# Kernel optimization log

Hardware: AMD Instinct MI355X
Metric: run time of the kernel (lower is better)

## Reference

```python
import jax, jax.numpy as jnp
import numpy as np

N, M = 8192, 4096
SCALE = 1e-4  # keeps tss ~ O(1) so the gaussian score doesn't underflow


def setup_inputs() -> dict:
    key = jax.random.key(0)
    x = jax.random.normal(key, (N, M), dtype=jnp.float32) * SCALE
    variance = jnp.asarray(0.9, dtype=jnp.float32)
    return {"x": x, "variance": variance}


def reference(x, variance):
    # _lpd vectorized over all columns at once.
    # series_a/series_b are first differences with a leading zero row; the
    # leading zeros contribute 0 to the sum (0*0>=0 -> 0-0), so we can work
    # directly on the diffs.
    d = jnp.diff(x, axis=0)                 # [N-1, M]
    da = d[:, :1]                           # reference column diffs [N-1, 1]
    db = d[:, 1:]                           # other column diffs    [N-1, M-1]
    diff = da - db
    hpdd = jnp.where(da * db >= 0, diff, jnp.abs(diff))
    tss = jnp.sum(hpdd, axis=0)             # [M-1]
    # torch.tensor(self.tss) detaches tss from x's autograd graph
    tss = jax.lax.stop_gradient(tss)

    # gaussian score with mean 0, sigma = variance
    sqrt_2pi = jnp.sqrt(jnp.asarray(2.0 * np.pi, dtype=x.dtype))
    coef = 1.0 / (sqrt_2pi * variance)
    score = coef * jnp.exp(-(tss ** 2) / (2.0 * variance ** 2))  # [M-1]

    # tan-softmax weighting
    t = jnp.tan(score)
    w = t / jnp.sum(t)                      # [M-1]

    y = jnp.reshape(jnp.sum(w * x[:, 1:]), (-1,))  # [1]
    return y
```

## Files before the change

kernel.cpp:

```cpp
#include <hip/hip_runtime.h>
#include <math.h>

#define NROWS 8192
#define NCOLS 4096
#define RPC 64
#define NCHUNK (NROWS / RPC)
#define TPB 256
#define CPT 4
#define CTILE (TPB * CPT)
#define NTILE (NCOLS / CTILE)
#define F2BLK 64
#define CPB2 (NCOLS / F2BLK)

typedef float f32x4 __attribute__((ext_vector_type(4)));

__global__ __launch_bounds__(TPB) void tss_partial_kernel(
    const float* __restrict__ x,
    float* __restrict__ ptss,
    float* __restrict__ pcs)
{
    const int tid   = threadIdx.x;
    const int tile  = blockIdx.x;
    const int chunk = blockIdx.y;
    const int col   = tile * CTILE + tid * CPT;
    const int r0    = chunk * RPC;

    __shared__ float x0[RPC + 1];
    __shared__ float da_sh[RPC];

    if (tid <= RPC) {
        int r = min(r0 + tid, NROWS - 1);
        x0[tid] = x[(size_t)r * NCOLS];
    }
    __syncthreads();
    if (tid < RPC) {
        da_sh[tid] = (r0 + tid + 1 < NROWS) ? (x0[tid + 1] - x0[tid]) : 0.0f;
    }
    __syncthreads();

    const f32x4* row = (const f32x4*)(x + (size_t)r0 * NCOLS + col);
    const int rs = NCOLS / 4;
    const int maxoff = NROWS - 1 - r0;

    float tss0 = 0.f, tss1 = 0.f, tss2 = 0.f, tss3 = 0.f;
    float cs0 = 0.f, cs1 = 0.f, cs2 = 0.f, cs3 = 0.f;

    f32x4 cur = row[0];
    f32x4 nxt = row[rs];

    #pragma unroll 8
    for (int i = 0; i < RPC; ++i) {
        const int offc = (i + 2 <= RPC) ? (i + 2) : RPC;
        const int off  = min(offc, maxoff);
        f32x4 pf = row[off * rs];

        cs0 += cur.x; cs1 += cur.y; cs2 += cur.z; cs3 += cur.w;

        const float da = da_sh[i];
        float db, df;
        db = nxt.x - cur.x; df = da - db;
        tss0 += (da * db >= 0.f) ? df : fabsf(df);
        db = nxt.y - cur.y; df = da - db;
        tss1 += (da * db >= 0.f) ? df : fabsf(df);
        db = nxt.z - cur.z; df = da - db;
        tss2 += (da * db >= 0.f) ? df : fabsf(df);
        db = nxt.w - cur.w; df = da - db;
        tss3 += (da * db >= 0.f) ? df : fabsf(df);

        cur = nxt;
        nxt = pf;
    }

    float* pt = ptss + (size_t)chunk * NCOLS + col;
    float* pc = pcs  + (size_t)chunk * NCOLS + col;
    pt[0] = tss0; pt[1] = tss1; pt[2] = tss2; pt[3] = tss3;
    pc[0] = cs0;  pc[1] = cs1;  pc[2] = cs2;  pc[3] = cs3;
}

__global__ __launch_bounds__(256) void tss_finalize_kernel(
    const float* __restrict__ ptss,
    const float* __restrict__ pcs,
    const float* __restrict__ variance,
    double* __restrict__ blk)
{
    const int tid  = threadIdx.x;
    const int part = tid >> 6;
    const int cpos = tid & 63;
    const int j    = blockIdx.x * CPB2 + cpos;

    double tss = 0.0, cs = 0.0;
    #pragma unroll 8
    for (int c = part * (NCHUNK / 4); c < (part + 1) * (NCHUNK / 4); ++c) {
        tss += (double)ptss[(size_t)c * NCOLS + j];
        cs  += (double)pcs[(size_t)c * NCOLS + j];
    }

    __shared__ double stss[4][CPB2];
    __shared__ double scs[4][CPB2];
    stss[part][cpos] = tss;
    scs[part][cpos]  = cs;
    __syncthreads();

    if (tid < 64) {
        tss = stss[0][cpos] + stss[1][cpos] + stss[2][cpos] + stss[3][cpos];
        cs  = scs[0][cpos] + scs[1][cpos] + scs[2][cpos] + scs[3][cpos];

        double t = 0.0, tc = 0.0;
        if (j >= 1) {
            const double var = (double)variance[0];
            const double SQRT_2PI = 2.5066282746310005024;
            const double coef = 1.0 / (SQRT_2PI * var);
            const double score = coef * exp(-(tss * tss) / (2.0 * var * var));
            t  = tan(score);
            tc = t * cs;
        }
        for (int o = 32; o > 0; o >>= 1) {
            t  += __shfl_down(t, o);
            tc += __shfl_down(tc, o);
        }
        if (cpos == 0) {
            blk[2 * blockIdx.x]     = t;
            blk[2 * blockIdx.x + 1] = tc;
        }
    }
}

__global__ __launch_bounds__(64) void tss_reduce_kernel(
    const double* __restrict__ blk,
    float* __restrict__ out)
{
    const int tid = threadIdx.x;
    double st  = blk[2 * tid];
    double stc = blk[2 * tid + 1];
    for (int o = 32; o > 0; o >>= 1) {
        st  += __shfl_down(st, o);
        stc += __shfl_down(stc, o);
    }
    if (tid == 0) out[0] = (float)(stc / st);
}

extern "C" void kernel_launch(void* const* d_in, const int* in_sizes, int n_in,
                              void* d_out, int out_size, void* d_ws, size_t ws_size,
                              hipStream_t stream) {
    const float* x   = (const float*)d_in[0];
    const float* var = (const float*)d_in[1];
    float* out = (float*)d_out;

    float* ptss = (float*)d_ws;
    float* pcs  = ptss + (size_t)NCHUNK * NCOLS;
    double* blk = (double*)(pcs + (size_t)NCHUNK * NCOLS);

    dim3 g1(NTILE, NCHUNK);
    tss_partial_kernel<<<g1, TPB, 0, stream>>>(x, ptss, pcs);
    tss_finalize_kernel<<<F2BLK, 256, 0, stream>>>(ptss, pcs, var, blk);
    tss_reduce_kernel<<<1, 64, 0, stream>>>(blk, out);
}
```

Measured before the change: 37.60 us.

## Use full-width 1024-thread row blocks with 32-row chunks and widen finalize

The partial kernel now launches one 1024-thread block per 32-row chunk that covers all 4096 columns, replacing the 2D grid of 256-thread column tiles over 64-row chunks. The reference-column diffs are then loaded once per chunk rather than once per tile. The finalize kernel moves to 128 blocks with 8 partial-sum groups and a shared-memory tree reduction, and the last kernel folds 128 block results. Halving the rows per chunk doubles the partial-sum buffer that finalize must read back, and the shorter per-thread loop leaves less latency hiding.

```diff
diff --git a/kernel.cpp b/kernel.cpp
--- a/kernel.cpp
+++ b/kernel.cpp
@@ -3,14 +3,13 @@
 
 #define NROWS 8192
 #define NCOLS 4096
-#define RPC 64
+#define RPC 32
 #define NCHUNK (NROWS / RPC)
-#define TPB 256
+#define TPB 1024
 #define CPT 4
-#define CTILE (TPB * CPT)
-#define NTILE (NCOLS / CTILE)
-#define F2BLK 64
+#define F2BLK 128
 #define CPB2 (NCOLS / F2BLK)
+#define PARTS 8
 
 typedef float f32x4 __attribute__((ext_vector_type(4)));
 
@@ -20,9 +19,8 @@
     float* __restrict__ pcs)
 {
     const int tid   = threadIdx.x;
-    const int tile  = blockIdx.x;
-    const int chunk = blockIdx.y;
-    const int col   = tile * CTILE + tid * CPT;
+    const int chunk = blockIdx.x;
+    const int col   = tid * CPT;
     const int r0    = chunk * RPC;
 
     __shared__ float x0[RPC + 1];
@@ -46,7 +44,7 @@
     float cs0 = 0.f, cs1 = 0.f, cs2 = 0.f, cs3 = 0.f;
 
     f32x4 cur = row[0];
-    f32x4 nxt = row[rs];
+    f32x4 nxt = row[min(1, maxoff) * rs];
 
     #pragma unroll 8
     for (int i = 0; i < RPC; ++i) {
@@ -84,29 +82,33 @@
     double* __restrict__ blk)
 {
     const int tid  = threadIdx.x;
-    const int part = tid >> 6;
-    const int cpos = tid & 63;
+    const int part = tid >> 5;
+    const int cpos = tid & 31;
     const int j    = blockIdx.x * CPB2 + cpos;
 
     double tss = 0.0, cs = 0.0;
     #pragma unroll 8
-    for (int c = part * (NCHUNK / 4); c < (part + 1) * (NCHUNK / 4); ++c) {
+    for (int c = part * (NCHUNK / PARTS); c < (part + 1) * (NCHUNK / PARTS); ++c) {
         tss += (double)ptss[(size_t)c * NCOLS + j];
         cs  += (double)pcs[(size_t)c * NCOLS + j];
     }
 
-    __shared__ double stss[4][CPB2];
-    __shared__ double scs[4][CPB2];
+    __shared__ double stss[PARTS][CPB2];
+    __shared__ double scs[PARTS][CPB2];
     stss[part][cpos] = tss;
     scs[part][cpos]  = cs;
     __syncthreads();
 
-    if (tid < 64) {
-        tss = stss[0][cpos] + stss[1][cpos] + stss[2][cpos] + stss[3][cpos];
-        cs  = scs[0][cpos] + scs[1][cpos] + scs[2][cpos] + scs[3][cpos];
+    __shared__ double s1[CPB2];
+    __shared__ double s2[CPB2];
+    if (tid < CPB2) {
+        tss = 0.0; cs = 0.0;
+        #pragma unroll
+        for (int p = 0; p < PARTS; ++p) { tss += stss[p][tid]; cs += scs[p][tid]; }
 
         double t = 0.0, tc = 0.0;
-        if (j >= 1) {
+        const int jj = blockIdx.x * CPB2 + tid;
+        if (jj >= 1) {
             const double var = (double)variance[0];
             const double SQRT_2PI = 2.5066282746310005024;
             const double coef = 1.0 / (SQRT_2PI * var);
@@ -114,14 +116,16 @@
             t  = tan(score);
             tc = t * cs;
         }
-        for (int o = 32; o > 0; o >>= 1) {
-            t  += __shfl_down(t, o);
-            tc += __shfl_down(tc, o);
-        }
-        if (cpos == 0) {
-            blk[2 * blockIdx.x]     = t;
-            blk[2 * blockIdx.x + 1] = tc;
-        }
+        s1[tid] = t; s2[tid] = tc;
+    }
+    __syncthreads();
+    for (int s = CPB2 / 2; s > 0; s >>= 1) {
+        if (tid < s) { s1[tid] += s1[tid + s]; s2[tid] += s2[tid + s]; }
+        __syncthreads();
+    }
+    if (tid == 0) {
+        blk[2 * blockIdx.x]     = s1[0];
+        blk[2 * blockIdx.x + 1] = s2[0];
     }
 }
 
@@ -130,8 +134,8 @@
     float* __restrict__ out)
 {
     const int tid = threadIdx.x;
-    double st  = blk[2 * tid];
-    double stc = blk[2 * tid + 1];
+    double st  = blk[2 * tid]     + blk[2 * (tid + 64)];
+    double stc = blk[2 * tid + 1] + blk[2 * (tid + 64) + 1];
     for (int o = 32; o > 0; o >>= 1) {
         st  += __shfl_down(st, o);
         stc += __shfl_down(stc, o);
@@ -150,8 +154,7 @@
     float* pcs  = ptss + (size_t)NCHUNK * NCOLS;
     double* blk = (double*)(pcs + (size_t)NCHUNK * NCOLS);
 
-    dim3 g1(NTILE, NCHUNK);
-    tss_partial_kernel<<<g1, TPB, 0, stream>>>(x, ptss, pcs);
+    tss_partial_kernel<<<NCHUNK, TPB, 0, stream>>>(x, ptss, pcs);
     tss_finalize_kernel<<<F2BLK, 256, 0, stream>>>(ptss, pcs, var, blk);
     tss_reduce_kernel<<<1, 64, 0, stream>>>(blk, out);
 }
```

Result: faster. 32.54 us (-13.5%).
